# Performance work log

Measured on AMD Instinct MI355X. Metric: run time of the kernel, lower is better.

## Reference

```python
import jax, jax.numpy as jnp
import numpy as np

ALPHA = 0.5  # mixing weight between dot-product and wedge-norm terms


def setup_inputs() -> dict:
    key = jax.random.key(0)
    kq, kk, kv = jax.random.split(key, 3)
    B, L, H, E = 2, 2048, 8, 32
    queries = jax.random.normal(kq, (B, L, H, E), dtype=jnp.float32)
    keys = jax.random.normal(kk, (B, L, H, E), dtype=jnp.float32)
    values = jax.random.normal(kv, (B, L, H, E), dtype=jnp.float32)
    return {"queries": queries, "keys": keys, "values": values}


def reference(queries, keys, values):
    # queries: [B,L,H,E], keys: [B,S,H,E], values: [B,S,H,D]
    E = queries.shape[-1]
    scale = 1.0 / jnp.sqrt(jnp.asarray(E, dtype=queries.dtype))
    # dot product scores: [B,H,L,S]
    dot = jnp.einsum('blhe,bshe->bhls', queries, keys)
    # squared norms -> broadcastable [B,H,L,1] and [B,H,1,S]
    qn2 = jnp.sum(queries ** 2, axis=-1).transpose(0, 2, 1)[..., :, None]
    kn2 = jnp.sum(keys ** 2, axis=-1).transpose(0, 2, 1)[..., None, :]
    # wedge (Clifford) squared norm, clamped at 0
    wedge = jax.nn.relu(qn2 * kn2 - dot ** 2)
    scores = (ALPHA * dot - (1.0 - ALPHA) * wedge) * scale
    attn = jax.nn.softmax(scores, axis=-1)  # [B,H,L,S]
    # out: [B,L,H,D]
    out = jnp.einsum('bhls,bshd->blhd', attn, values)
    return out
```

## Files before the change

### kernel.cpp

```cpp
#include <hip/hip_runtime.h>
#include <hip/hip_bf16.h>
#include <math.h>


#define NB 2
#define NL 2048
#define NS 2048
#define NH 8
#define NBH 16
#define CSC 0.12751742f

#define WS_KN2_OFF 0u
#define WS_KHKL_OFF 131072u
#define WS_VT_OFF (131072u + 4194304u)
#define WS_PACC_OFF (131072u + 4194304u + 2097152u)
#define WS_PML_OFF (WS_PACC_OFF + 16777216u)
#define WS_NEED (WS_PML_OFF + 1048576u)

typedef float f32x4 __attribute__((ext_vector_type(4)));
typedef short s16x8 __attribute__((ext_vector_type(8)));
typedef unsigned short u16;

__device__ inline unsigned pk2(float a, float b) {
    __hip_bfloat162 t = __float22bfloat162_rn(make_float2(a, b));
    union { __hip_bfloat162 h; unsigned u; } cv;
    cv.h = t;
    return cv.u;
}
template <int CTRL>
__device__ inline float dpp_add(float x) {
    return x + __int_as_float(__builtin_amdgcn_mov_dpp(__float_as_int(x), CTRL, 0xF, 0xF, false));
}
__device__ inline void dma16(const void* gp, void* lp) {
    __builtin_amdgcn_global_load_lds(
        (__attribute__((address_space(1))) void*)(void*)gp,
        (__attribute__((address_space(3))) void*)lp, 16, 0, 0);
}
__device__ inline int swzK(int row) { return (row ^ (row >> 2)) & 3; }
__device__ inline int swzV(int row) { return (row + (row >> 3)) & 7; }

__global__ __launch_bounds__(256) void ga_pre(const float* __restrict__ K,
                                              const float* __restrict__ V,
                                              float* __restrict__ kn2w,
                                              u16* __restrict__ khkl,
                                              u16* __restrict__ vtw) {
    __shared__ float Vf[64][36];
    const int T = threadIdx.x;
    const int bh = blockIdx.x >> 5, stile = blockIdx.x & 31;
    const int b = bh >> 3, h = bh & 7;
    const int s0 = stile * 64;
    const int sk = T >> 2, kc = T & 3;

    const float* kp = K + ((size_t)((b * NS + s0 + sk) * NH + h)) * 32 + kc * 8;
    float4 f0 = *(const float4*)kp, f1 = *(const float4*)(kp + 4);
    float kx[8] = {f0.x, f0.y, f0.z, f0.w, f1.x, f1.y, f1.z, f1.w};
    unsigned hh[4], ll[4];
    float kn2p = 0.f;
#pragma unroll
    for (int i = 0; i < 4; i++) {
        float x0 = kx[2 * i], x1 = kx[2 * i + 1];
        kn2p = fmaf(x0, x0, kn2p);
        kn2p = fmaf(x1, x1, kn2p);
        unsigned h01 = pk2(x0, x1);
        hh[i] = h01;
        float h0 = __uint_as_float(h01 << 16);
        float h1 = __uint_as_float(h01 & 0xffff0000u);
        ll[i] = pk2(x0 - h0, x1 - h1);
    }
    u16* kd = khkl + ((size_t)(bh * NS + s0 + sk)) * 64;
    const int swk = sk & 7;
    *(uint4*)(kd + ((kc ^ swk) * 8)) = make_uint4(hh[0], hh[1], hh[2], hh[3]);
    *(uint4*)(kd + (((4 + kc) ^ swk) * 8)) = make_uint4(ll[0], ll[1], ll[2], ll[3]);
    kn2p = dpp_add<0xB1>(kn2p);
    kn2p = dpp_add<0x4E>(kn2p);
    if (kc == 0) kn2w[bh * NS + s0 + sk] = kn2p;

    const float* vp = V + ((size_t)((b * NS + s0 + sk) * NH + h)) * 32 + kc * 8;
    float4 g0 = *(const float4*)vp, g1 = *(const float4*)(vp + 4);
    *(float4*)&Vf[sk][kc * 8] = g0;
    *(float4*)&Vf[sk][kc * 8 + 4] = g1;
    __syncthreads();
    const int dr = T >> 3, c = T & 7;
    float vv[8];
#pragma unroll
    for (int i = 0; i < 8; i++) vv[i] = Vf[c * 8 + i][dr];
    const int phys = c ^ (dr & 7);
    *(uint4*)(vtw + ((size_t)(bh * 32 + dr)) * NS + s0 + phys * 8) =
        make_uint4(pk2(vv[0], vv[1]), pk2(vv[2], vv[3]), pk2(vv[4], vv[5]), pk2(vv[6], vv[7]));
}

__global__ __launch_bounds__(256, 4) void ga_dma(
    const float* __restrict__ Q, const float* __restrict__ kn2w,
    const u16* __restrict__ khkl, const u16* __restrict__ vtw,
    float* __restrict__ pacc, float* __restrict__ pml) {
    __shared__ u16 sK[2][64][64];
    __shared__ u16 sV[2][32][64];
    __shared__ u16 sP[4][16][64];

    const int T = threadIdx.x;
    const int lane = T & 63, wave = T >> 6;
    const int g = lane >> 4, lc = lane & 15, g8 = g * 8;
    const int blk = blockIdx.x;
    const int qt = blk & 31, strip = (blk >> 5) & 3, bh = blk >> 7;
    const int b = bh >> 3, h = bh & 7;
    const int qw = qt * 64 + wave * 16;
    const int kb0 = strip * 512;

    const float* qrow = Q + ((size_t)((b * NL + qw + lc) * NH + h)) * 32 + g8;
    float4 qa = *(const float4*)qrow, qb = *(const float4*)(qrow + 4);
    float q8[8] = {qa.x, qa.y, qa.z, qa.w, qb.x, qb.y, qb.z, qb.w};
    union { unsigned u4[4]; s16x8 v; } qh_, ql_;
    float qn2 = 0.f;
#pragma unroll
    for (int i = 0; i < 4; i++) {
        float x0 = q8[2 * i], x1 = q8[2 * i + 1];
        qn2 = fmaf(x0, x0, qn2);
        qn2 = fmaf(x1, x1, qn2);
        unsigned h01 = pk2(x0, x1);
        qh_.u4[i] = h01;
        float h0 = __uint_as_float(h01 << 16);
        float h1 = __uint_as_float(h01 & 0xffff0000u);
        ql_.u4[i] = pk2(x0 - h0, x1 - h1);
    }
    const s16x8 qh = qh_.v, ql = ql_.v;
    qn2 += __shfl_xor(qn2, 16);
    qn2 += __shfl_xor(qn2, 32);

    const char* ksrc = (const char*)khkl +
        ((size_t)(bh * NS + kb0 + 16 * wave)) * 128 + lane * 16;
    const char* vsrc = (const char*)vtw +
        ((size_t)(bh * 32 + 8 * wave + (lane >> 3))) * (NS * 2) +
        (size_t)(kb0 + (lane & 7) * 8) * 2;
    const float* kn2b = kn2w + (size_t)bh * NS + kb0;

    dma16(ksrc, &sK[0][16 * wave][0]);
    dma16(ksrc + 1024, &sK[0][16 * wave + 8][0]);
    dma16(vsrc, &sV[0][8 * wave][0]);
    __syncthreads();

    s16x8 ones;
#pragma unroll
    for (int i = 0; i < 8; i++) ones[i] = (short)0x3F80;

    f32x4 acc0 = {0.f, 0.f, 0.f, 0.f}, acc1 = {0.f, 0.f, 0.f, 0.f};
    float m = -1e30f, l = 0.f;
    const f32x4 z = {0.f, 0.f, 0.f, 0.f};
    const int sw = lc & 7;

    for (int t = 0; t < 8; ++t) {
        const int cur = t & 1;
        if (t + 1 < 8) {
            const char* k2 = ksrc + (size_t)(t + 1) * 8192;
            const char* v2 = vsrc + (size_t)(t + 1) * 128;
            dma16(k2, &sK[cur ^ 1][16 * wave][0]);
            dma16(k2 + 1024, &sK[cur ^ 1][16 * wave + 8][0]);
            dma16(v2, &sV[cur ^ 1][8 * wave][0]);
        }
        const int kl64 = t * 64;

        f32x4 d[4], kn2v[4];
#pragma unroll
        for (int st = 0; st < 4; st++) {
            kn2v[st] = *(const f32x4*)(kn2b + kl64 + 16 * st + 4 * g);
            s16x8 kh = *(s16x8*)&sK[cur][16 * st + lc][(g ^ sw) * 8];
            s16x8 klo = *(s16x8*)&sK[cur][16 * st + lc][((4 + g) ^ sw) * 8];
            f32x4 dd = __builtin_amdgcn_mfma_f32_16x16x32_bf16(klo, qh, z, 0, 0, 0);
            dd = __builtin_amdgcn_mfma_f32_16x16x32_bf16(kh, ql, dd, 0, 0, 0);
            dd = __builtin_amdgcn_mfma_f32_16x16x32_bf16(kh, qh, dd, 0, 0, 0);
            d[st] = dd;
        }
        s16x8 va0 = *(s16x8*)&sV[cur][lc][(g ^ sw) * 8];
        s16x8 va1 = *(s16x8*)&sV[cur][lc][((4 + g) ^ sw) * 8];
        s16x8 va2 = *(s16x8*)&sV[cur][lc + 16][(g ^ sw) * 8];
        s16x8 va3 = *(s16x8*)&sV[cur][lc + 16][((4 + g) ^ sw) * 8];

        float sc[4][4];
#pragma unroll
        for (int st = 0; st < 4; st++)
#pragma unroll
            for (int r = 0; r < 4; r++) {
                float dd = d[st][r];
                float c = qn2 * kn2v[st][r];
                sc[st][r] = fminf(dd, fmaf(dd, dd, -c) + dd);
            }

        float x0 = fmaxf(fmaxf(sc[0][0], sc[0][1]), fmaxf(sc[0][2], sc[0][3]));
        float x1 = fmaxf(fmaxf(sc[1][0], sc[1][1]), fmaxf(sc[1][2], sc[1][3]));
        float x2 = fmaxf(fmaxf(sc[2][0], sc[2][1]), fmaxf(sc[2][2], sc[2][3]));
        float x3 = fmaxf(fmaxf(sc[3][0], sc[3][1]), fmaxf(sc[3][2], sc[3][3]));
        float tm = fmaxf(fmaxf(x0, x1), fmaxf(x2, x3));
        tm = fmaxf(tm, __shfl_xor(tm, 16));
        tm = fmaxf(tm, __shfl_xor(tm, 32));
        const float nm = fmaxf(m, tm);
        const float negmC = -nm * CSC;
        const float al = __builtin_amdgcn_exp2f(fmaf(m, CSC, negmC));
        m = nm;
        float p[4][4];
#pragma unroll
        for (int st = 0; st < 4; st++)
#pragma unroll
            for (int r = 0; r < 4; r++)
                p[st][r] = __builtin_amdgcn_exp2f(fmaf(sc[st][r], CSC, negmC));

#pragma unroll
        for (int st = 0; st < 4; st++) {
            const int off = (((2 * st + (g >> 1)) ^ sw) << 3) + ((g & 1) << 2);
            *(uint2*)&sP[wave][lc][off] =
                make_uint2(pk2(p[st][0], p[st][1]), pk2(p[st][2], p[st][3]));
        }
        __builtin_amdgcn_s_waitcnt(0xC07F);
        s16x8 pb0 = *(s16x8*)&sP[wave][lc][(g ^ sw) * 8];
        s16x8 pb1 = *(s16x8*)&sP[wave][lc][((4 + g) ^ sw) * 8];

        acc0 *= al;
        acc1 *= al;
        acc0 = __builtin_amdgcn_mfma_f32_16x16x32_bf16(va0, pb0, acc0, 0, 0, 0);
        acc0 = __builtin_amdgcn_mfma_f32_16x16x32_bf16(va1, pb1, acc0, 0, 0, 0);
        acc1 = __builtin_amdgcn_mfma_f32_16x16x32_bf16(va2, pb0, acc1, 0, 0, 0);
        acc1 = __builtin_amdgcn_mfma_f32_16x16x32_bf16(va3, pb1, acc1, 0, 0, 0);
        f32x4 lt = __builtin_amdgcn_mfma_f32_16x16x32_bf16(ones, pb0, z, 0, 0, 0);
        lt = __builtin_amdgcn_mfma_f32_16x16x32_bf16(ones, pb1, lt, 0, 0, 0);
        l = fmaf(l, al, lt[0]);

        __syncthreads();
    }

    float* pa = pacc + (((size_t)bh * 4 + strip) * NL + (qw + lc)) * 32;
    *(f32x4*)(pa + 4 * g) = acc0;
    *(f32x4*)(pa + 16 + 4 * g) = acc1;
    if (g == 0) {
        *(float2*)(pml + (((size_t)bh * 4 + strip) * NL + (qw + lc)) * 2) =
            make_float2(m, l);
    }
}

__global__ __launch_bounds__(256) void ga_combine(const float* __restrict__ pacc,
                                                  const float* __restrict__ pml,
                                                  float* __restrict__ O) {
    const int tid = blockIdx.x * 256 + threadIdx.x;
    const int dq = tid & 7, q = (tid >> 3) & 2047, bh = tid >> 14;
    const int b = bh >> 3, h = bh & 7;
    float m[4], l[4];
#pragma unroll
    for (int s = 0; s < 4; s++) {
        float2 t = *(const float2*)(pml + (((size_t)bh * 4 + s) * NL + q) * 2);
        m[s] = t.x;
        l[s] = t.y;
    }
    float mf = fmaxf(fmaxf(m[0], m[1]), fmaxf(m[2], m[3]));
    float w[4], L = 0.f;
#pragma unroll
    for (int s = 0; s < 4; s++) {
        w[s] = __builtin_amdgcn_exp2f((m[s] - mf) * CSC);
        L = fmaf(l[s], w[s], L);
    }
    const float inv = 1.f / L;
    float4 o = make_float4(0.f, 0.f, 0.f, 0.f);
#pragma unroll
    for (int s = 0; s < 4; s++) {
        const float* pa = pacc + (((size_t)bh * 4 + s) * NL + q) * 32 + dq * 4;
        float4 a = *(const float4*)pa;
        o.x = fmaf(a.x, w[s], o.x);
        o.y = fmaf(a.y, w[s], o.y);
        o.z = fmaf(a.z, w[s], o.z);
        o.w = fmaf(a.w, w[s], o.w);
    }
    o.x *= inv; o.y *= inv; o.z *= inv; o.w *= inv;
    *(float4*)(O + (((size_t)(b * NL + q)) * NH + h) * 32 + dq * 4) = o;
}

__global__ __launch_bounds__(512, 4) void ga_fallback(
    const float* __restrict__ Q, const float* __restrict__ K,
    const float* __restrict__ V, float* __restrict__ O) {
    __shared__ union {
        struct {
            u16 Kh[2][64][32];
            u16 Kl[2][64][32];
            u16 Vt[2][32][64];
            float kn2[2][64];
        } s;
        struct { float acc[8][32][17]; float m[8][16]; float l[8][16]; } c;
    } u;
    __shared__ u16 sP[8][16][64];

    const int T = threadIdx.x;
    const int lane = T & 63, wave = T >> 6;
    const int g = lane >> 4, lc = lane & 15, g8 = g * 8;
    const int half = wave >> 2;
    const int qt = blockIdx.x & 31;
    const int bh = blockIdx.x >> 5;
    const int b = bh >> 3, h = bh & 7;
    const int qw = qt * 64 + (wave & 3) * 16;

    const float* qrow = Q + ((size_t)((b * NL + qw + lc) * NH + h)) * 32 + g8;
    float4 qa = *(const float4*)qrow, qb = *(const float4*)(qrow + 4);
    float q8[8] = {qa.x, qa.y, qa.z, qa.w, qb.x, qb.y, qb.z, qb.w};
    union { unsigned u4[4]; s16x8 v; } qh_, ql_;
    float qn2 = 0.f;
#pragma unroll
    for (int i = 0; i < 4; i++) {
        float x0 = q8[2 * i], x1 = q8[2 * i + 1];
        qn2 = fmaf(x0, x0, qn2);
        qn2 = fmaf(x1, x1, qn2);
        unsigned h01 = pk2(x0, x1);
        qh_.u4[i] = h01;
        float h0 = __uint_as_float(h01 << 16);
        float h1 = __uint_as_float(h01 & 0xffff0000u);
        ql_.u4[i] = pk2(x0 - h0, x1 - h1);
    }
    const s16x8 qh = qh_.v, ql = ql_.v;
    qn2 += __shfl_xor(qn2, 16);
    qn2 += __shfl_xor(qn2, 32);

    const int Tl = T & 255;
    const int sk = Tl >> 2, kc = Tl & 3;
    const int dv = Tl & 31, vc = Tl >> 5;
    const float* kbase = K + ((size_t)(b * NS * NH) + h) * 32;
    const float* vbase = V + ((size_t)(b * NS * NH) + h) * 32;
    const int kphys = (kc ^ swzK(sk)) * 8;
    const int vphys = (vc ^ swzV(dv)) * 8;

    int s0 = half * 1024;
    float4 ka = *(const float4*)(kbase + (size_t)(s0 + sk) * 256 + kc * 8);
    float4 kb = *(const float4*)(kbase + (size_t)(s0 + sk) * 256 + kc * 8 + 4);
    float vr[8];
#pragma unroll
    for (int i = 0; i < 8; i++) vr[i] = vbase[(size_t)(s0 + 8 * vc + i) * 256 + dv];

    f32x4 acc0 = {0.f, 0.f, 0.f, 0.f}, acc1 = {0.f, 0.f, 0.f, 0.f};
    float m = -INFINITY, l = 0.f;

    for (int t = 0; t < 16; ++t) {
        {
            float kx[8] = {ka.x, ka.y, ka.z, ka.w, kb.x, kb.y, kb.z, kb.w};
            unsigned hh[4], ll[4];
            float kn2p = 0.f;
#pragma unroll
            for (int i = 0; i < 4; i++) {
                float x0 = kx[2 * i], x1 = kx[2 * i + 1];
                kn2p = fmaf(x0, x0, kn2p);
                kn2p = fmaf(x1, x1, kn2p);
                unsigned h01 = pk2(x0, x1);
                hh[i] = h01;
                float h0 = __uint_as_float(h01 << 16);
                float h1 = __uint_as_float(h01 & 0xffff0000u);
                ll[i] = pk2(x0 - h0, x1 - h1);
            }
            *(uint4*)&u.s.Kh[half][sk][kphys] = make_uint4(hh[0], hh[1], hh[2], hh[3]);
            *(uint4*)&u.s.Kl[half][sk][kphys] = make_uint4(ll[0], ll[1], ll[2], ll[3]);
            kn2p = dpp_add<0xB1>(kn2p);
            kn2p = dpp_add<0x4E>(kn2p);
            if (kc == 0) u.s.kn2[half][sk] = kn2p;
            *(uint4*)&u.s.Vt[half][dv][vphys] =
                make_uint4(pk2(vr[0], vr[1]), pk2(vr[2], vr[3]),
                           pk2(vr[4], vr[5]), pk2(vr[6], vr[7]));
        }
        const int tn = (t + 1 < 16) ? t + 1 : t;
        const int sn = half * 1024 + tn * 64;
        ka = *(const float4*)(kbase + (size_t)(sn + sk) * 256 + kc * 8);
        kb = *(const float4*)(kbase + (size_t)(sn + sk) * 256 + kc * 8 + 4);
#pragma unroll
        for (int i = 0; i < 8; i++) vr[i] = vbase[(size_t)(sn + 8 * vc + i) * 256 + dv];

        __syncthreads();

        f32x4 d[4], kn2v[4];
        const f32x4 z = {0.f, 0.f, 0.f, 0.f};
        const int skr = swzK(lc);
#pragma unroll
        for (int st = 0; st < 4; st++) {
            kn2v[st] = *(f32x4*)&u.s.kn2[half][16 * st + 4 * g];
            s16x8 kh = *(s16x8*)&u.s.Kh[half][16 * st + lc][(g ^ skr) * 8];
            s16x8 kl = *(s16x8*)&u.s.Kl[half][16 * st + lc][(g ^ skr) * 8];
            f32x4 dd = __builtin_amdgcn_mfma_f32_16x16x32_bf16(kl, qh, z, 0, 0, 0);
            dd = __builtin_amdgcn_mfma_f32_16x16x32_bf16(kh, ql, dd, 0, 0, 0);
            dd = __builtin_amdgcn_mfma_f32_16x16x32_bf16(kh, qh, dd, 0, 0, 0);
            d[st] = dd;
        }

        float sc[4][4];
#pragma unroll
        for (int st = 0; st < 4; st++)
#pragma unroll
            for (int r = 0; r < 4; r++) {
                float dd = d[st][r];
                float w = fmaxf(fmaf(-dd, dd, qn2 * kn2v[st][r]), 0.f);
                sc[st][r] = (dd - w) * CSC;
            }

        float x0 = fmaxf(fmaxf(sc[0][0], sc[0][1]), fmaxf(sc[0][2], sc[0][3]));
        float x1 = fmaxf(fmaxf(sc[1][0], sc[1][1]), fmaxf(sc[1][2], sc[1][3]));
        float x2 = fmaxf(fmaxf(sc[2][0], sc[2][1]), fmaxf(sc[2][2], sc[2][3]));
        float x3 = fmaxf(fmaxf(sc[3][0], sc[3][1]), fmaxf(sc[3][2], sc[3][3]));
        float tm = fmaxf(fmaxf(x0, x1), fmaxf(x2, x3));
        tm = fmaxf(tm, __shfl_xor(tm, 16));
        tm = fmaxf(tm, __shfl_xor(tm, 32));
        const float nm = fmaxf(m, tm);
        const float al = __builtin_amdgcn_exp2f(m - nm);
        m = nm;
        float p[4][4], ls = 0.f;
#pragma unroll
        for (int st = 0; st < 4; st++)
#pragma unroll
            for (int r = 0; r < 4; r++) {
                p[st][r] = __builtin_amdgcn_exp2f(sc[st][r] - nm);
                ls += p[st][r];
            }
        l = fmaf(l, al, ls);
        acc0 *= al;
        acc1 *= al;

#pragma unroll
        for (int st = 0; st < 4; st++) {
            const int off = ((2 * st + (g >> 1)) ^ (lc & 7)) * 8 + (g & 1) * 4;
            *(uint2*)&sP[wave][lc][off] =
                make_uint2(pk2(p[st][0], p[st][1]), pk2(p[st][2], p[st][3]));
        }
        __builtin_amdgcn_s_waitcnt(0xC07F);

        const int svl = swzV(lc), svh = swzV(lc + 16), spl = lc & 7;
        s16x8 va00 = *(s16x8*)&u.s.Vt[half][lc][(g ^ svl) * 8];
        s16x8 va01 = *(s16x8*)&u.s.Vt[half][lc][((4 + g) ^ svl) * 8];
        s16x8 va10 = *(s16x8*)&u.s.Vt[half][lc + 16][(g ^ svh) * 8];
        s16x8 va11 = *(s16x8*)&u.s.Vt[half][lc + 16][((4 + g) ^ svh) * 8];
        s16x8 pb0 = *(s16x8*)&sP[wave][lc][(g ^ spl) * 8];
        s16x8 pb1 = *(s16x8*)&sP[wave][lc][((4 + g) ^ spl) * 8];
        acc0 = __builtin_amdgcn_mfma_f32_16x16x32_bf16(va00, pb0, acc0, 0, 0, 0);
        acc0 = __builtin_amdgcn_mfma_f32_16x16x32_bf16(va01, pb1, acc0, 0, 0, 0);
        acc1 = __builtin_amdgcn_mfma_f32_16x16x32_bf16(va10, pb0, acc1, 0, 0, 0);
        acc1 = __builtin_amdgcn_mfma_f32_16x16x32_bf16(va11, pb1, acc1, 0, 0, 0);

        __syncthreads();
    }

    l += __shfl_xor(l, 16);
    l += __shfl_xor(l, 32);
#pragma unroll
    for (int r = 0; r < 4; r++) {
        u.c.acc[wave][4 * g + r][lc] = acc0[r];
        u.c.acc[wave][16 + 4 * g + r][lc] = acc1[r];
    }
    if (lane < 16) {
        u.c.m[wave][lc] = m;
        u.c.l[wave][lc] = l;
    }
    __syncthreads();

    const int q = T >> 3, dq = (T & 7) * 4, qr = q & 15;
    const int w0 = q >> 4, w1 = w0 + 4;
    float m0 = u.c.m[w0][qr], m1 = u.c.m[w1][qr];
    float l0 = u.c.l[w0][qr], l1 = u.c.l[w1][qr];
    float mf = fmaxf(m0, m1);
    float e0 = __builtin_amdgcn_exp2f(m0 - mf);
    float e1 = __builtin_amdgcn_exp2f(m1 - mf);
    float inv = 1.f / fmaf(l1, e1, l0 * e0);
    e0 *= inv;
    e1 *= inv;
    float4 o;
    o.x = u.c.acc[w0][dq + 0][qr] * e0 + u.c.acc[w1][dq + 0][qr] * e1;
    o.y = u.c.acc[w0][dq + 1][qr] * e0 + u.c.acc[w1][dq + 1][qr] * e1;
    o.z = u.c.acc[w0][dq + 2][qr] * e0 + u.c.acc[w1][dq + 2][qr] * e1;
    o.w = u.c.acc[w0][dq + 3][qr] * e0 + u.c.acc[w1][dq + 3][qr] * e1;
    *(float4*)(O + ((size_t)((b * NL + qt * 64 + q) * NH + h)) * 32 + dq) = o;
}

extern "C" void kernel_launch(void* const* d_in, const int* in_sizes, int n_in,
                              void* d_out, int out_size, void* d_ws, size_t ws_size,
                              hipStream_t stream) {
    const float* Q = (const float*)d_in[0];
    const float* K = (const float*)d_in[1];
    const float* V = (const float*)d_in[2];
    float* O = (float*)d_out;

    if (ws_size >= (size_t)WS_NEED) {
        float* kn2w = (float*)((char*)d_ws + WS_KN2_OFF);
        u16* khkl = (u16*)((char*)d_ws + WS_KHKL_OFF);
        u16* vtw = (u16*)((char*)d_ws + WS_VT_OFF);
        float* pacc = (float*)((char*)d_ws + WS_PACC_OFF);
        float* pml = (float*)((char*)d_ws + WS_PML_OFF);
        ga_pre<<<NBH * 32, 256, 0, stream>>>(K, V, kn2w, khkl, vtw);
        ga_dma<<<NBH * 32 * 4, 256, 0, stream>>>(Q, kn2w, khkl, vtw, pacc, pml);
        ga_combine<<<(NBH * NL * 8) / 256, 256, 0, stream>>>(pacc, pml, O);
    } else {
        ga_fallback<<<NBH * 32, 512, 0, stream>>>(Q, K, V, O);
    }
}
```

Measured before the change: 106.2 us.

## Rework attention main loop with register-permuted P, deferred rescale, and tile-blocked V layout

The main kernel now uses 32-key tiles with smaller LDS buffers and a higher occupancy hint. The P matrix is passed to the PV MFMA through permlane swaps instead of an LDS round trip, and the ones-MFMA row sum is replaced by a per-lane scalar sum. The online-softmax rescale is skipped unless the running max grows past a threshold. The preprocessing kernel writes V^T in a tile-blocked, swizzled layout to match. Block order is also changed so that query tiles vary slowest. These changes aim to cut LDS traffic, MFMA count and serial dependencies, at the cost of more loop iterations and more synchronizations.

```diff
diff --git a/kernel.cpp b/kernel.cpp
--- a/kernel.cpp
+++ b/kernel.cpp
@@ -8,7 +8,10 @@
 #define NS 2048
 #define NH 8
 #define NBH 16
+#define STRIPS 4
+#define NT 16
 #define CSC 0.12751742f
+#define DEFER_THR 24.0f
 
 #define WS_KN2_OFF 0u
 #define WS_KHKL_OFF 131072u
@@ -18,6 +21,7 @@
 #define WS_NEED (WS_PML_OFF + 1048576u)
 
 typedef float f32x4 __attribute__((ext_vector_type(4)));
+typedef float f32x2 __attribute__((ext_vector_type(2)));
 typedef short s16x8 __attribute__((ext_vector_type(8)));
 typedef unsigned short u16;
 
@@ -35,6 +39,12 @@
     __builtin_amdgcn_global_load_lds(
         (__attribute__((address_space(1))) void*)(void*)gp,
         (__attribute__((address_space(3))) void*)lp, 16, 0, 0);
+}
+__device__ inline void pl32(unsigned& a, unsigned& b) {
+    asm("v_permlane32_swap_b32 %0, %1" : "+v"(a), "+v"(b));
+}
+__device__ inline void pl16(unsigned& a, unsigned& b) {
+    asm("v_permlane16_swap_b32 %0, %1" : "+v"(a), "+v"(b));
 }
 __device__ inline int swzK(int row) { return (row ^ (row >> 2)) & 3; }
 __device__ inline int swzV(int row) { return (row + (row >> 3)) & 7; }
@@ -77,31 +87,35 @@
 
     const float* vp = V + ((size_t)((b * NS + s0 + sk) * NH + h)) * 32 + kc * 8;
     float4 g0 = *(const float4*)vp, g1 = *(const float4*)(vp + 4);
-    *(float4*)&Vf[sk][kc * 8] = g0;
-    *(float4*)&Vf[sk][kc * 8 + 4] = g1;
+    const int chv = kc ^ ((sk >> 3) & 3);
+    *(float4*)&Vf[sk][chv * 8] = g0;
+    *(float4*)&Vf[sk][chv * 8 + 4] = g1;
     __syncthreads();
     const int dr = T >> 3, c = T & 7;
     float vv[8];
 #pragma unroll
-    for (int i = 0; i < 8; i++) vv[i] = Vf[c * 8 + i][dr];
-    const int phys = c ^ (dr & 7);
-    *(uint4*)(vtw + ((size_t)(bh * 32 + dr)) * NS + s0 + phys * 8) =
+    for (int i = 0; i < 8; i++)
+        vv[i] = Vf[c * 8 + i][(((dr >> 3) ^ (c & 3)) << 3) + (dr & 7)];
+    const int tt = (s0 >> 5) + (c >> 2);
+    const int r = dr >> 1;
+    const int slot = ((dr & 1) << 2) + ((c & 3) ^ (r & 3));
+    *(uint4*)(vtw + (size_t)bh * 65536 + tt * 1024 + r * 64 + slot * 8) =
         make_uint4(pk2(vv[0], vv[1]), pk2(vv[2], vv[3]), pk2(vv[4], vv[5]), pk2(vv[6], vv[7]));
 }
 
-__global__ __launch_bounds__(256, 4) void ga_dma(
+__global__ __launch_bounds__(256, 8) void ga_lean(
     const float* __restrict__ Q, const float* __restrict__ kn2w,
     const u16* __restrict__ khkl, const u16* __restrict__ vtw,
     float* __restrict__ pacc, float* __restrict__ pml) {
-    __shared__ u16 sK[2][64][64];
-    __shared__ u16 sV[2][32][64];
-    __shared__ u16 sP[4][16][64];
+    __shared__ u16 sK[2][32][64];
+    __shared__ u16 sV[2][16][64];
 
     const int T = threadIdx.x;
     const int lane = T & 63, wave = T >> 6;
     const int g = lane >> 4, lc = lane & 15, g8 = g * 8;
     const int blk = blockIdx.x;
-    const int qt = blk & 31, strip = (blk >> 5) & 3, bh = blk >> 7;
+    const int qt = blk >> 6, grp = blk & 63;
+    const int bh = grp >> 2, strip = grp & 3;
     const int b = bh >> 3, h = bh & 7;
     const int qw = qt * 64 + wave * 16;
     const int kb0 = strip * 512;
@@ -126,110 +140,117 @@
     qn2 += __shfl_xor(qn2, 16);
     qn2 += __shfl_xor(qn2, 32);
 
-    const char* ksrc = (const char*)khkl +
-        ((size_t)(bh * NS + kb0 + 16 * wave)) * 128 + lane * 16;
-    const char* vsrc = (const char*)vtw +
-        ((size_t)(bh * 32 + 8 * wave + (lane >> 3))) * (NS * 2) +
-        (size_t)(kb0 + (lane & 7) * 8) * 2;
-    const float* kn2b = kn2w + (size_t)bh * NS + kb0;
-
-    dma16(ksrc, &sK[0][16 * wave][0]);
-    dma16(ksrc + 1024, &sK[0][16 * wave + 8][0]);
-    dma16(vsrc, &sV[0][8 * wave][0]);
+    const char* ksrc = (const char*)khkl + ((size_t)(bh * NS + kb0 + 8 * wave)) * 128 + lane * 16;
+    const char* vsrc = (const char*)vtw + ((size_t)bh * 65536 + (kb0 >> 5) * 1024) * 2 +
+                       wave * 1024 + lane * 16;
+    const float* knb = kn2w + (size_t)bh * NS + kb0 + 4 * g;
+
+    dma16(ksrc, &sK[0][8 * wave][0]);
+    if (wave < 2) dma16(vsrc, &sV[0][8 * wave][0]);
     __syncthreads();
-
-    s16x8 ones;
-#pragma unroll
-    for (int i = 0; i < 8; i++) ones[i] = (short)0x3F80;
 
     f32x4 acc0 = {0.f, 0.f, 0.f, 0.f}, acc1 = {0.f, 0.f, 0.f, 0.f};
     float m = -1e30f, l = 0.f;
     const f32x4 z = {0.f, 0.f, 0.f, 0.f};
     const int sw = lc & 7;
-
-    for (int t = 0; t < 8; ++t) {
+    const int vslot = ((lc & 1) << 2) + (g ^ ((lc >> 1) & 3));
+
+#pragma unroll 1
+    for (int t = 0; t < NT; ++t) {
         const int cur = t & 1;
-        if (t + 1 < 8) {
-            const char* k2 = ksrc + (size_t)(t + 1) * 8192;
-            const char* v2 = vsrc + (size_t)(t + 1) * 128;
-            dma16(k2, &sK[cur ^ 1][16 * wave][0]);
-            dma16(k2 + 1024, &sK[cur ^ 1][16 * wave + 8][0]);
-            dma16(v2, &sV[cur ^ 1][8 * wave][0]);
-        }
-        const int kl64 = t * 64;
-
-        f32x4 d[4], kn2v[4];
-#pragma unroll
-        for (int st = 0; st < 4; st++) {
-            kn2v[st] = *(const f32x4*)(kn2b + kl64 + 16 * st + 4 * g);
-            s16x8 kh = *(s16x8*)&sK[cur][16 * st + lc][(g ^ sw) * 8];
-            s16x8 klo = *(s16x8*)&sK[cur][16 * st + lc][((4 + g) ^ sw) * 8];
-            f32x4 dd = __builtin_amdgcn_mfma_f32_16x16x32_bf16(klo, qh, z, 0, 0, 0);
+        if (t + 1 < NT) {
+            dma16(ksrc + (size_t)(t + 1) * 4096, &sK[cur ^ 1][8 * wave][0]);
+            if (wave < 2) dma16(vsrc + (size_t)(t + 1) * 2048, &sV[cur ^ 1][8 * wave][0]);
+        }
+
+        f32x4 d0, d1;
+        {
+            s16x8 kh = *(s16x8*)&sK[cur][lc][(g ^ sw) * 8];
+            s16x8 kl = *(s16x8*)&sK[cur][lc][((4 + g) ^ sw) * 8];
+            f32x4 dd = __builtin_amdgcn_mfma_f32_16x16x32_bf16(kl, qh, z, 0, 0, 0);
             dd = __builtin_amdgcn_mfma_f32_16x16x32_bf16(kh, ql, dd, 0, 0, 0);
-            dd = __builtin_amdgcn_mfma_f32_16x16x32_bf16(kh, qh, dd, 0, 0, 0);
-            d[st] = dd;
-        }
-        s16x8 va0 = *(s16x8*)&sV[cur][lc][(g ^ sw) * 8];
-        s16x8 va1 = *(s16x8*)&sV[cur][lc][((4 + g) ^ sw) * 8];
-        s16x8 va2 = *(s16x8*)&sV[cur][lc + 16][(g ^ sw) * 8];
-        s16x8 va3 = *(s16x8*)&sV[cur][lc + 16][((4 + g) ^ sw) * 8];
-
-        float sc[4][4];
-#pragma unroll
-        for (int st = 0; st < 4; st++)
-#pragma unroll
-            for (int r = 0; r < 4; r++) {
-                float dd = d[st][r];
-                float c = qn2 * kn2v[st][r];
-                sc[st][r] = fminf(dd, fmaf(dd, dd, -c) + dd);
+            d0 = __builtin_amdgcn_mfma_f32_16x16x32_bf16(kh, qh, dd, 0, 0, 0);
+        }
+        {
+            s16x8 kh = *(s16x8*)&sK[cur][16 + lc][(g ^ sw) * 8];
+            s16x8 kl = *(s16x8*)&sK[cur][16 + lc][((4 + g) ^ sw) * 8];
+            f32x4 dd = __builtin_amdgcn_mfma_f32_16x16x32_bf16(kl, qh, z, 0, 0, 0);
+            dd = __builtin_amdgcn_mfma_f32_16x16x32_bf16(kh, ql, dd, 0, 0, 0);
+            d1 = __builtin_amdgcn_mfma_f32_16x16x32_bf16(kh, qh, dd, 0, 0, 0);
+        }
+        f32x4 kn20 = *(const f32x4*)(knb + t * 32);
+        f32x4 kn21 = *(const f32x4*)(knb + t * 32 + 16);
+
+        float sc[2][4];
+        {
+            const f32x2 q2 = {qn2, qn2};
+            f32x4 dm[2] = {d0, d1};
+            f32x4 km[2] = {kn20, kn21};
+#pragma unroll
+            for (int st = 0; st < 2; st++) {
+                f32x2 kk0 = {km[st][0], km[st][1]}, kk1 = {km[st][2], km[st][3]};
+                f32x2 dd0 = {dm[st][0], dm[st][1]}, dd1 = {dm[st][2], dm[st][3]};
+                f32x2 e0 = dd0 - q2 * kk0;
+                f32x2 e1 = dd1 - q2 * kk1;
+                f32x2 t0 = dd0 * dd0 + e0;
+                f32x2 t1 = dd1 * dd1 + e1;
+                sc[st][0] = fminf(dm[st][0], t0[0]);
+                sc[st][1] = fminf(dm[st][1], t0[1]);
+                sc[st][2] = fminf(dm[st][2], t1[0]);
+                sc[st][3] = fminf(dm[st][3], t1[1]);
             }
-
-        float x0 = fmaxf(fmaxf(sc[0][0], sc[0][1]), fmaxf(sc[0][2], sc[0][3]));
-        float x1 = fmaxf(fmaxf(sc[1][0], sc[1][1]), fmaxf(sc[1][2], sc[1][3]));
-        float x2 = fmaxf(fmaxf(sc[2][0], sc[2][1]), fmaxf(sc[2][2], sc[2][3]));
-        float x3 = fmaxf(fmaxf(sc[3][0], sc[3][1]), fmaxf(sc[3][2], sc[3][3]));
-        float tm = fmaxf(fmaxf(x0, x1), fmaxf(x2, x3));
-        tm = fmaxf(tm, __shfl_xor(tm, 16));
-        tm = fmaxf(tm, __shfl_xor(tm, 32));
-        const float nm = fmaxf(m, tm);
-        const float negmC = -nm * CSC;
-        const float al = __builtin_amdgcn_exp2f(fmaf(m, CSC, negmC));
-        m = nm;
-        float p[4][4];
-#pragma unroll
-        for (int st = 0; st < 4; st++)
-#pragma unroll
-            for (int r = 0; r < 4; r++)
-                p[st][r] = __builtin_amdgcn_exp2f(fmaf(sc[st][r], CSC, negmC));
-
-#pragma unroll
-        for (int st = 0; st < 4; st++) {
-            const int off = (((2 * st + (g >> 1)) ^ sw) << 3) + ((g & 1) << 2);
-            *(uint2*)&sP[wave][lc][off] =
-                make_uint2(pk2(p[st][0], p[st][1]), pk2(p[st][2], p[st][3]));
-        }
-        __builtin_amdgcn_s_waitcnt(0xC07F);
-        s16x8 pb0 = *(s16x8*)&sP[wave][lc][(g ^ sw) * 8];
-        s16x8 pb1 = *(s16x8*)&sP[wave][lc][((4 + g) ^ sw) * 8];
-
-        acc0 *= al;
-        acc1 *= al;
-        acc0 = __builtin_amdgcn_mfma_f32_16x16x32_bf16(va0, pb0, acc0, 0, 0, 0);
-        acc0 = __builtin_amdgcn_mfma_f32_16x16x32_bf16(va1, pb1, acc0, 0, 0, 0);
-        acc1 = __builtin_amdgcn_mfma_f32_16x16x32_bf16(va2, pb0, acc1, 0, 0, 0);
-        acc1 = __builtin_amdgcn_mfma_f32_16x16x32_bf16(va3, pb1, acc1, 0, 0, 0);
-        f32x4 lt = __builtin_amdgcn_mfma_f32_16x16x32_bf16(ones, pb0, z, 0, 0, 0);
-        lt = __builtin_amdgcn_mfma_f32_16x16x32_bf16(ones, pb1, lt, 0, 0, 0);
-        l = fmaf(l, al, lt[0]);
+        }
+
+        float tm = fmaxf(fmaxf(fmaxf(sc[0][0], sc[0][1]), fmaxf(sc[0][2], sc[0][3])),
+                         fmaxf(fmaxf(sc[1][0], sc[1][1]), fmaxf(sc[1][2], sc[1][3])));
+        if (!__all(tm <= m + DEFER_THR)) {
+            tm = fmaxf(tm, __shfl_xor(tm, 16));
+            tm = fmaxf(tm, __shfl_xor(tm, 32));
+            const float nm = fmaxf(m, tm);
+            const float al = __builtin_amdgcn_exp2f((m - nm) * CSC);
+            m = nm;
+            acc0 *= al;
+            acc1 *= al;
+            l *= al;
+        }
+        const float negmC = -m * CSC;
+        const f32x2 cscv = {CSC, CSC}, nmv = {negmC, negmC};
+        float p[2][4];
+#pragma unroll
+        for (int st = 0; st < 2; st++) {
+            f32x2 s0 = {sc[st][0], sc[st][1]}, s1 = {sc[st][2], sc[st][3]};
+            f32x2 e0 = s0 * cscv + nmv;
+            f32x2 e1 = s1 * cscv + nmv;
+            p[st][0] = __builtin_amdgcn_exp2f(e0[0]);
+            p[st][1] = __builtin_amdgcn_exp2f(e0[1]);
+            p[st][2] = __builtin_amdgcn_exp2f(e1[0]);
+            p[st][3] = __builtin_amdgcn_exp2f(e1[1]);
+        }
+        l += ((p[0][0] + p[0][1]) + (p[0][2] + p[0][3])) +
+             ((p[1][0] + p[1][1]) + (p[1][2] + p[1][3]));
+
+        unsigned w00 = pk2(p[0][0], p[0][1]), w01 = pk2(p[0][2], p[0][3]);
+        unsigned w10 = pk2(p[1][0], p[1][1]), w11 = pk2(p[1][2], p[1][3]);
+        pl32(w00, w10); pl32(w01, w11);
+        pl16(w00, w10); pl16(w01, w11);
+        union { uint4 u; s16x8 v; } P;
+        P.u = make_uint4(w00, w01, w10, w11);
+
+        s16x8 vlo = *(s16x8*)&sV[cur][lc >> 1][vslot * 8];
+        s16x8 vhi = *(s16x8*)&sV[cur][8 + (lc >> 1)][vslot * 8];
+        acc0 = __builtin_amdgcn_mfma_f32_16x16x32_bf16(vlo, P.v, acc0, 0, 0, 0);
+        acc1 = __builtin_amdgcn_mfma_f32_16x16x32_bf16(vhi, P.v, acc1, 0, 0, 0);
 
         __syncthreads();
     }
 
-    float* pa = pacc + (((size_t)bh * 4 + strip) * NL + (qw + lc)) * 32;
+    l += __shfl_xor(l, 16);
+    l += __shfl_xor(l, 32);
+    float* pa = pacc + (((size_t)bh * STRIPS + strip) * NL + (qw + lc)) * 32;
     *(f32x4*)(pa + 4 * g) = acc0;
     *(f32x4*)(pa + 16 + 4 * g) = acc1;
     if (g == 0) {
-        *(float2*)(pml + (((size_t)bh * 4 + strip) * NL + (qw + lc)) * 2) =
+        *(float2*)(pml + (((size_t)bh * STRIPS + strip) * NL + (qw + lc)) * 2) =
             make_float2(m, l);
     }
 }
@@ -243,7 +264,7 @@
     float m[4], l[4];
 #pragma unroll
     for (int s = 0; s < 4; s++) {
-        float2 t = *(const float2*)(pml + (((size_t)bh * 4 + s) * NL + q) * 2);
+        float2 t = *(const float2*)(pml + (((size_t)bh * STRIPS + s) * NL + q) * 2);
         m[s] = t.x;
         l[s] = t.y;
     }
@@ -258,7 +279,7 @@
     float4 o = make_float4(0.f, 0.f, 0.f, 0.f);
 #pragma unroll
     for (int s = 0; s < 4; s++) {
-        const float* pa = pacc + (((size_t)bh * 4 + s) * NL + q) * 32 + dq * 4;
+        const float* pa = pacc + (((size_t)bh * STRIPS + s) * NL + q) * 32 + dq * 4;
         float4 a = *(const float4*)pa;
         o.x = fmaf(a.x, w[s], o.x);
         o.y = fmaf(a.y, w[s], o.y);
@@ -479,7 +500,7 @@
         float* pacc = (float*)((char*)d_ws + WS_PACC_OFF);
         float* pml = (float*)((char*)d_ws + WS_PML_OFF);
         ga_pre<<<NBH * 32, 256, 0, stream>>>(K, V, kn2w, khkl, vtw);
-        ga_dma<<<NBH * 32 * 4, 256, 0, stream>>>(Q, kn2w, khkl, vtw, pacc, pml);
+        ga_lean<<<NBH * 32 * STRIPS, 256, 0, stream>>>(Q, kn2w, khkl, vtw, pacc, pml);
         ga_combine<<<(NBH * NL * 8) / 256, 256, 0, stream>>>(pacc, pml, O);
     } else {
         ga_fallback<<<NBH * 32, 512, 0, stream>>>(Q, K, V, O);
```

New measurement: 106.3 us. About the same (+0.1%).
